# Kernel tuning notes

Hardware: AMD Instinct MI355X
Metric: run time of the kernel (lower is better)

## Reference

```python
import jax, jax.numpy as jnp
import numpy as np

N = 100000   # nodes
E = 3200000  # edges (avg degree 32)
D_IN = 512
D_OUT = 512


def setup_inputs() -> dict:
    key = jax.random.key(0)
    k1, k2, k3, k4, k5 = jax.random.split(key, 5)
    features = jax.random.normal(k1, (N, D_IN), dtype=jnp.float32)
    # Glorot-uniform-like init for the dense weight
    limit = float(np.sqrt(6.0 / (D_IN + D_OUT)))
    weight = jax.random.uniform(k2, (D_IN, D_OUT), dtype=jnp.float32, minval=-limit, maxval=limit)
    rows = jax.random.randint(k3, (E,), 0, N, dtype=jnp.int64)  # destination node per edge
    cols = jax.random.randint(k4, (E,), 0, N, dtype=jnp.int64)  # source node per edge
    vals = jax.random.uniform(k5, (E,), dtype=jnp.float32)      # adjacency edge weights
    return {"features": features, "weight": weight, "rows": rows, "cols": cols, "vals": vals}


def reference(features, weight, rows, cols, vals):
    # support = features @ W  (dense projection)
    support = features @ weight                       # [N, D_OUT]
    # sparse_dense_matmul(adj, support): out[i] = sum_e vals[e] * support[cols[e]] for rows[e]==i
    msgs = vals[:, None] * support[cols]              # [E, D_OUT] gather + scale
    out = jax.ops.segment_sum(msgs, rows, num_segments=N)  # scatter-add aggregate
    # final=False branch -> ReLU
    return jax.nn.relu(out)
```

## Files before the change

kernel.cpp:

```cpp
#include <hip/hip_runtime.h>
#include <cstdint>
#include <cstddef>

#define NN 100000
#define NE 3200000
#define DD 512

typedef __attribute__((ext_vector_type(4))) float f32x4;
typedef __attribute__((ext_vector_type(8))) __bf16 bf16x8;
typedef __attribute__((ext_vector_type(8))) unsigned short u16x8;
typedef __attribute__((ext_vector_type(4))) unsigned short u16x4;

__device__ __forceinline__ unsigned short f2bf(float x) {
    unsigned u = __builtin_bit_cast(unsigned, x);
    u = (u + 0x7FFFu + ((u >> 16) & 1u)) >> 16;
    return (unsigned short)u;
}
__device__ __forceinline__ float bf2f(unsigned short x) {
    unsigned u = ((unsigned)x) << 16;
    return __builtin_bit_cast(float, u);
}

__global__ __launch_bounds__(256) void wtr_kernel(const float* __restrict__ W,
                                                  unsigned short* __restrict__ Bt) {
    __shared__ unsigned short tile[64][65];
    int t = threadIdx.x;
    int bn = blockIdx.x & 7;
    int bk = blockIdx.x >> 3;
    #pragma unroll
    for (int i = 0; i < 16; ++i) {
        int flat = i * 256 + t;
        int r = flat >> 6, c = flat & 63;
        tile[r][c] = f2bf(W[(size_t)(bk * 64 + r) * DD + bn * 64 + c]);
    }
    __syncthreads();
    #pragma unroll
    for (int i = 0; i < 16; ++i) {
        int flat = i * 256 + t;
        int r = flat >> 6, c = flat & 63;
        Bt[(size_t)(bn * 64 + r) * DD + bk * 64 + c] = tile[c][r];
    }
}

__global__ __launch_bounds__(256) void hist_kernel(const int* __restrict__ rows,
                                                   int* __restrict__ cnt) {
    int i = blockIdx.x * 256 + threadIdx.x;
    if (i < NE) atomicAdd(&cnt[rows[i]], 1);
}

__global__ __launch_bounds__(1024) void scan_kernel(const int* __restrict__ cnt,
                                                    int* __restrict__ rs) {
    __shared__ int lds[1024];
    int t = threadIdx.x;
    const int per = (NN + 1023) / 1024;
    int b = t * per; if (b > NN) b = NN;
    int e = b + per; if (e > NN) e = NN;
    int s = 0;
    for (int i = b; i < e; ++i) s += cnt[i];
    lds[t] = s;
    __syncthreads();
    for (int off = 1; off < 1024; off <<= 1) {
        int u = (t >= off) ? lds[t - off] : 0;
        __syncthreads();
        lds[t] += u;
        __syncthreads();
    }
    int run = lds[t] - s;
    for (int i = b; i < e; ++i) { rs[i] = run; run += cnt[i]; }
    if (t == 1023) rs[NN] = lds[1023];
}

__global__ __launch_bounds__(256) void scatter_kernel(const int* __restrict__ rows,
                                                      const int* __restrict__ cols,
                                                      const float* __restrict__ vals,
                                                      const int* __restrict__ rs,
                                                      int* __restrict__ cur,
                                                      int2* __restrict__ ed) {
    int i = blockIdx.x * 256 + threadIdx.x;
    if (i < NE) {
        int r = rows[i];
        int p = rs[r] + atomicAdd(&cur[r], 1);
        ed[p] = make_int2(cols[i], __float_as_int(vals[i]));
    }
}

__global__ __launch_bounds__(256) void gemm_kernel(const float* __restrict__ A,
                                                   const unsigned short* __restrict__ Bt,
                                                   unsigned short* __restrict__ S) {
    __shared__ unsigned short sA[128 * 40];
    __shared__ unsigned short sB[128 * 40];
    const int tid = threadIdx.x;
    const int lane = tid & 63;
    const int w = tid >> 6;
    const int wm = w >> 1, wn = w & 1;
    const int row0 = blockIdx.x * 128;
    const int n0 = blockIdx.y * 128;
    const int kg = lane >> 4;
    const int r16 = lane & 15;

    f32x4 acc[4][4] = {};

    for (int kt = 0; kt < DD / 32; ++kt) {
        const int k0 = kt * 32;
        __syncthreads();
        #pragma unroll
        for (int i = 0; i < 4; ++i) {
            int f = i * 256 + tid;
            int r = f >> 3;
            int kq = f & 7;
            int gr = row0 + r;
            float4 v = make_float4(0.f, 0.f, 0.f, 0.f);
            if (gr < NN) v = *reinterpret_cast<const float4*>(&A[(size_t)gr * DD + k0 + kq * 4]);
            u16x4 bv;
            bv[0] = f2bf(v.x); bv[1] = f2bf(v.y); bv[2] = f2bf(v.z); bv[3] = f2bf(v.w);
            *reinterpret_cast<u16x4*>(&sA[r * 40 + kq * 4]) = bv;
        }
        #pragma unroll
        for (int i = 0; i < 2; ++i) {
            int c = i * 256 + tid;
            int n = c >> 2;
            int kq = c & 3;
            u16x8 v = *reinterpret_cast<const u16x8*>(&Bt[(size_t)(n0 + n) * DD + k0 + kq * 8]);
            *reinterpret_cast<u16x8*>(&sB[n * 40 + kq * 8]) = v;
        }
        __syncthreads();
        bf16x8 af[4], bfv[4];
        #pragma unroll
        for (int mi = 0; mi < 4; ++mi)
            af[mi] = *reinterpret_cast<const bf16x8*>(&sA[(wm * 64 + mi * 16 + r16) * 40 + kg * 8]);
        #pragma unroll
        for (int ni = 0; ni < 4; ++ni)
            bfv[ni] = *reinterpret_cast<const bf16x8*>(&sB[(wn * 64 + ni * 16 + r16) * 40 + kg * 8]);
        #pragma unroll
        for (int mi = 0; mi < 4; ++mi)
            #pragma unroll
            for (int ni = 0; ni < 4; ++ni)
                acc[mi][ni] = __builtin_amdgcn_mfma_f32_16x16x32_bf16(af[mi], bfv[ni], acc[mi][ni], 0, 0, 0);
    }

    const int cg = lane >> 4;
    const int cl = lane & 15;
    #pragma unroll
    for (int mi = 0; mi < 4; ++mi) {
        #pragma unroll
        for (int ni = 0; ni < 4; ++ni) {
            #pragma unroll
            for (int r = 0; r < 4; ++r) {
                int row = row0 + wm * 64 + mi * 16 + cg * 4 + r;
                if (row < NN)
                    S[(size_t)row * DD + n0 + wn * 64 + ni * 16 + cl] = f2bf(acc[mi][ni][r]);
            }
        }
    }
}

__global__ __launch_bounds__(256) void agg_kernel(const unsigned short* __restrict__ S,
                                                  const int2* __restrict__ ed,
                                                  const int* __restrict__ rs,
                                                  float* __restrict__ out) {
    int node = blockIdx.x * 4 + (threadIdx.x >> 6);
    if (node >= NN) return;
    int lane = threadIdx.x & 63;
    int beg = rs[node], end = rs[node + 1];
    float acc[8] = {0.f, 0.f, 0.f, 0.f, 0.f, 0.f, 0.f, 0.f};
    int e = beg;
    for (; e + 4 <= end; e += 4) {
        int2 e0 = ed[e], e1 = ed[e + 1], e2 = ed[e + 2], e3 = ed[e + 3];
        u16x8 s0 = *reinterpret_cast<const u16x8*>(&S[(size_t)e0.x * DD + lane * 8]);
        u16x8 s1 = *reinterpret_cast<const u16x8*>(&S[(size_t)e1.x * DD + lane * 8]);
        u16x8 s2 = *reinterpret_cast<const u16x8*>(&S[(size_t)e2.x * DD + lane * 8]);
        u16x8 s3 = *reinterpret_cast<const u16x8*>(&S[(size_t)e3.x * DD + lane * 8]);
        float v0 = __int_as_float(e0.y), v1 = __int_as_float(e1.y);
        float v2 = __int_as_float(e2.y), v3 = __int_as_float(e3.y);
        #pragma unroll
        for (int j = 0; j < 8; ++j) {
            acc[j] += v0 * bf2f(s0[j]);
            acc[j] += v1 * bf2f(s1[j]);
            acc[j] += v2 * bf2f(s2[j]);
            acc[j] += v3 * bf2f(s3[j]);
        }
    }
    for (; e < end; ++e) {
        int2 e0 = ed[e];
        u16x8 s0 = *reinterpret_cast<const u16x8*>(&S[(size_t)e0.x * DD + lane * 8]);
        float v0 = __int_as_float(e0.y);
        #pragma unroll
        for (int j = 0; j < 8; ++j) acc[j] += v0 * bf2f(s0[j]);
    }
    f32x4 o0, o1;
    #pragma unroll
    for (int j = 0; j < 4; ++j) {
        o0[j] = fmaxf(acc[j], 0.f);
        o1[j] = fmaxf(acc[4 + j], 0.f);
    }
    size_t base = (size_t)node * DD + (size_t)lane * 8;
    *reinterpret_cast<f32x4*>(&out[base]) = o0;
    *reinterpret_cast<f32x4*>(&out[base + 4]) = o1;
}

extern "C" void kernel_launch(void* const* d_in, const int* in_sizes, int n_in,
                              void* d_out, int out_size, void* d_ws, size_t ws_size,
                              hipStream_t stream) {
    const float* feat = (const float*)d_in[0];
    const float* wgt  = (const float*)d_in[1];
    const int*   rows = (const int*)d_in[2];
    const int*   cols = (const int*)d_in[3];
    const float* vals = (const float*)d_in[4];
    float* out = (float*)d_out;

    char* ws = (char*)d_ws;
    size_t off = 0;
    auto alloc = [&](size_t bytes) -> void* {
        void* p = (void*)(ws + off);
        off += (bytes + 255) & ~(size_t)255;
        return p;
    };
    unsigned short* support = (unsigned short*)alloc((size_t)NN * DD * 2);
    unsigned short* Bt      = (unsigned short*)alloc((size_t)DD * DD * 2);
    int* cnt  = (int*)alloc((size_t)NN * 4);
    int* rsv  = (int*)alloc((size_t)(NN + 1) * 4);
    int* cur  = (int*)alloc((size_t)NN * 4);
    int2* ed  = (int2*)alloc((size_t)NE * 8);

    hipMemsetAsync(cnt, 0, (size_t)NN * 4, stream);
    hipMemsetAsync(cur, 0, (size_t)NN * 4, stream);

    wtr_kernel<<<64, 256, 0, stream>>>(wgt, Bt);
    hist_kernel<<<(NE + 255) / 256, 256, 0, stream>>>(rows, cnt);
    scan_kernel<<<1, 1024, 0, stream>>>(cnt, rsv);
    scatter_kernel<<<(NE + 255) / 256, 256, 0, stream>>>(rows, cols, vals, rsv, cur, ed);
    gemm_kernel<<<dim3((NN + 127) / 128, DD / 128), 256, 0, stream>>>(feat, Bt, support);
    agg_kernel<<<(NN + 3) / 4, 256, 0, stream>>>(support, ed, rsv, out);
}
```

Baseline: 1.378 ms.

## Vectorize CSR build, remap GEMM blocks for XCD locality, deepen aggregation prefetch

The histogram and scatter kernels now have each thread handle four edges through int4/float4 loads, so a quarter as many blocks are launched. The GEMM grid becomes 1D with a block-index remap that spreads work across 8 groups (391 blocks each), aiming for better L2 reuse of A rows per XCD. The aggregation loop issues eight gathered row loads before accumulating with fma, giving more memory-level parallelism, and the output is written with nontemporal stores. The remap constants and the vector loads are hardcoded to NN, NE and the edge count being a multiple of 4.

```diff
diff --git a/kernel.cpp b/kernel.cpp
--- a/kernel.cpp
+++ b/kernel.cpp
@@ -45,7 +45,11 @@
 __global__ __launch_bounds__(256) void hist_kernel(const int* __restrict__ rows,
                                                    int* __restrict__ cnt) {
     int i = blockIdx.x * 256 + threadIdx.x;
-    if (i < NE) atomicAdd(&cnt[rows[i]], 1);
+    int4 r4 = reinterpret_cast<const int4*>(rows)[i];
+    atomicAdd(&cnt[r4.x], 1);
+    atomicAdd(&cnt[r4.y], 1);
+    atomicAdd(&cnt[r4.z], 1);
+    atomicAdd(&cnt[r4.w], 1);
 }
 
 __global__ __launch_bounds__(1024) void scan_kernel(const int* __restrict__ cnt,
@@ -77,11 +81,14 @@
                                                       int* __restrict__ cur,
                                                       int2* __restrict__ ed) {
     int i = blockIdx.x * 256 + threadIdx.x;
-    if (i < NE) {
-        int r = rows[i];
-        int p = rs[r] + atomicAdd(&cur[r], 1);
-        ed[p] = make_int2(cols[i], __float_as_int(vals[i]));
-    }
+    int4 r4 = reinterpret_cast<const int4*>(rows)[i];
+    int4 c4 = reinterpret_cast<const int4*>(cols)[i];
+    float4 v4 = reinterpret_cast<const float4*>(vals)[i];
+    int p;
+    p = rs[r4.x] + atomicAdd(&cur[r4.x], 1); ed[p] = make_int2(c4.x, __float_as_int(v4.x));
+    p = rs[r4.y] + atomicAdd(&cur[r4.y], 1); ed[p] = make_int2(c4.y, __float_as_int(v4.y));
+    p = rs[r4.z] + atomicAdd(&cur[r4.z], 1); ed[p] = make_int2(c4.z, __float_as_int(v4.z));
+    p = rs[r4.w] + atomicAdd(&cur[r4.w], 1); ed[p] = make_int2(c4.w, __float_as_int(v4.w));
 }
 
 __global__ __launch_bounds__(256) void gemm_kernel(const float* __restrict__ A,
@@ -93,8 +100,10 @@
     const int lane = tid & 63;
     const int w = tid >> 6;
     const int wm = w >> 1, wn = w & 1;
-    const int row0 = blockIdx.x * 128;
-    const int n0 = blockIdx.y * 128;
+    const int bid = blockIdx.x;
+    const int wg = (bid & 7) * 391 + (bid >> 3);
+    const int row0 = (wg >> 2) * 128;
+    const int n0 = (wg & 3) * 128;
     const int kg = lane >> 4;
     const int r16 = lane & 15;
 
@@ -164,28 +173,27 @@
     int beg = rs[node], end = rs[node + 1];
     float acc[8] = {0.f, 0.f, 0.f, 0.f, 0.f, 0.f, 0.f, 0.f};
     int e = beg;
-    for (; e + 4 <= end; e += 4) {
-        int2 e0 = ed[e], e1 = ed[e + 1], e2 = ed[e + 2], e3 = ed[e + 3];
-        u16x8 s0 = *reinterpret_cast<const u16x8*>(&S[(size_t)e0.x * DD + lane * 8]);
-        u16x8 s1 = *reinterpret_cast<const u16x8*>(&S[(size_t)e1.x * DD + lane * 8]);
-        u16x8 s2 = *reinterpret_cast<const u16x8*>(&S[(size_t)e2.x * DD + lane * 8]);
-        u16x8 s3 = *reinterpret_cast<const u16x8*>(&S[(size_t)e3.x * DD + lane * 8]);
-        float v0 = __int_as_float(e0.y), v1 = __int_as_float(e1.y);
-        float v2 = __int_as_float(e2.y), v3 = __int_as_float(e3.y);
+    for (; e + 8 <= end; e += 8) {
+        u16x8 sv[8];
+        float vv[8];
         #pragma unroll
         for (int j = 0; j < 8; ++j) {
-            acc[j] += v0 * bf2f(s0[j]);
-            acc[j] += v1 * bf2f(s1[j]);
-            acc[j] += v2 * bf2f(s2[j]);
-            acc[j] += v3 * bf2f(s3[j]);
-        }
+            int2 ee = ed[e + j];
+            sv[j] = *reinterpret_cast<const u16x8*>(&S[(size_t)ee.x * DD + lane * 8]);
+            vv[j] = __int_as_float(ee.y);
+        }
+        #pragma unroll
+        for (int j = 0; j < 8; ++j)
+            #pragma unroll
+            for (int d = 0; d < 8; ++d)
+                acc[d] = fmaf(vv[j], bf2f(sv[j][d]), acc[d]);
     }
     for (; e < end; ++e) {
         int2 e0 = ed[e];
         u16x8 s0 = *reinterpret_cast<const u16x8*>(&S[(size_t)e0.x * DD + lane * 8]);
         float v0 = __int_as_float(e0.y);
         #pragma unroll
-        for (int j = 0; j < 8; ++j) acc[j] += v0 * bf2f(s0[j]);
+        for (int j = 0; j < 8; ++j) acc[j] = fmaf(v0, bf2f(s0[j]), acc[j]);
     }
     f32x4 o0, o1;
     #pragma unroll
@@ -194,8 +202,8 @@
         o1[j] = fmaxf(acc[4 + j], 0.f);
     }
     size_t base = (size_t)node * DD + (size_t)lane * 8;
-    *reinterpret_cast<f32x4*>(&out[base]) = o0;
-    *reinterpret_cast<f32x4*>(&out[base + 4]) = o1;
+    __builtin_nontemporal_store(o0, reinterpret_cast<f32x4*>(&out[base]));
+    __builtin_nontemporal_store(o1, reinterpret_cast<f32x4*>(&out[base + 4]));
 }
 
 extern "C" void kernel_launch(void* const* d_in, const int* in_sizes, int n_in,
@@ -226,9 +234,9 @@
     hipMemsetAsync(cur, 0, (size_t)NN * 4, stream);
 
     wtr_kernel<<<64, 256, 0, stream>>>(wgt, Bt);
-    hist_kernel<<<(NE + 255) / 256, 256, 0, stream>>>(rows, cnt);
+    hist_kernel<<<NE / 1024, 256, 0, stream>>>(rows, cnt);
     scan_kernel<<<1, 1024, 0, stream>>>(cnt, rsv);
-    scatter_kernel<<<(NE + 255) / 256, 256, 0, stream>>>(rows, cols, vals, rsv, cur, ed);
-    gemm_kernel<<<dim3((NN + 127) / 128, DD / 128), 256, 0, stream>>>(feat, Bt, support);
+    scatter_kernel<<<NE / 1024, 256, 0, stream>>>(rows, cols, vals, rsv, cur, ed);
+    gemm_kernel<<<3128, 256, 0, stream>>>(feat, Bt, support);
     agg_kernel<<<(NN + 3) / 4, 256, 0, stream>>>(support, ed, rsv, out);
 }
```

New measurement: 1.390 ms. About the same (+0.9%).
